# Kernel tuning notes

Measured on AMD Instinct MI355X. Metric: run time of the kernel, lower is better.

Reference implementation:

```python
import jax, jax.numpy as jnp
import numpy as np

BATCH = 16384
D = 4096  # input_features


def setup_inputs() -> dict:
    key = jax.random.key(0)
    k1, k2, k3 = jax.random.split(key, 3)
    x0 = jax.random.normal(k1, (BATCH, D), dtype=jnp.float32)
    x_cross = jax.random.normal(k2, (BATCH, D), dtype=jnp.float32)
    # RandomNormal(mean=0, stddev=sqrt(2/input_features))
    w = jax.random.normal(k3, (D,), dtype=jnp.float32) * np.float32(np.sqrt(2.0 / D))
    b = jnp.full((D,), 0.1, dtype=jnp.float32)
    return {"x0": x0, "x_cross": x_cross, "w": w, "b": b}


def reference(x0, x_cross, w, b):
    # Original: tensordot(x0[:, :, None] @ x_cross[:, None, :], w, [[-1],[0]]) + b + x_cross
    # Algebraically identical fused form (avoids the O(B*d^2) intermediate):
    #   x0 * (x_cross . w) + b + x_cross
    s = jnp.einsum("bd,d->b", x_cross, w)  # [B]
    return x0 * s[:, None] + b + x_cross
```

## Files before the change

kernel.cpp:

```cpp
#include <hip/hip_runtime.h>


constexpr int D_DIM = 4096;
constexpr int TPB   = 256;
constexpr int V4    = D_DIM / 4;
constexpr int F4PT  = V4 / TPB;

__global__ __launch_bounds__(TPB)
void cross_fused_kernel(const float* __restrict__ x0,
                        const float* __restrict__ xc,
                        const float* __restrict__ w,
                        const float* __restrict__ bias,
                        float* __restrict__ out) {
    const int row = blockIdx.x;
    const size_t base = (size_t)row * D_DIM;

    const float4* __restrict__ xc4  = (const float4*)(xc + base);
    const float4* __restrict__ x04  = (const float4*)(x0 + base);
    const float4* __restrict__ w4   = (const float4*)w;
    const float4* __restrict__ b4   = (const float4*)bias;
    float4* __restrict__       out4 = (float4*)(out + base);

    const int t = threadIdx.x;

    float4 xcv[F4PT];
    float partial = 0.0f;
#pragma unroll
    for (int i = 0; i < F4PT; ++i) {
        const int idx = t + i * TPB;
        xcv[i] = xc4[idx];
        const float4 wv = w4[idx];
        partial += xcv[i].x * wv.x + xcv[i].y * wv.y
                 + xcv[i].z * wv.z + xcv[i].w * wv.w;
    }

#pragma unroll
    for (int off = 32; off >= 1; off >>= 1)
        partial += __shfl_down(partial, off);

    __shared__ float wsum[TPB / 64];
    const int lane = t & 63, wid = t >> 6;
    if (lane == 0) wsum[wid] = partial;
    __syncthreads();
    const float s = wsum[0] + wsum[1] + wsum[2] + wsum[3];

#pragma unroll
    for (int i = 0; i < F4PT; ++i) {
        const int idx = t + i * TPB;
        const float4 x0v = x04[idx];
        const float4 bv  = b4[idx];
        float4 o;
        o.x = x0v.x * s + bv.x + xcv[i].x;
        o.y = x0v.y * s + bv.y + xcv[i].y;
        o.z = x0v.z * s + bv.z + xcv[i].z;
        o.w = x0v.w * s + bv.w + xcv[i].w;
        out4[idx] = o;
    }
}

extern "C" void kernel_launch(void* const* d_in, const int* in_sizes, int n_in,
                              void* d_out, int out_size, void* d_ws, size_t ws_size,
                              hipStream_t stream) {
    const float* x0   = (const float*)d_in[0];
    const float* xc   = (const float*)d_in[1];
    const float* w    = (const float*)d_in[2];
    const float* bias = (const float*)d_in[3];
    float* out        = (float*)d_out;

    const int rows = in_sizes[0] / D_DIM;
    cross_fused_kernel<<<rows, TPB, 0, stream>>>(x0, xc, w, bias, out);
}
```

Baseline: 141.0 us.

## Process multiple rows per block with double-buffered loads and nontemporal stores

Each block now handles eight rows and ping-pongs between two register buffers, issuing the next row's x_cross and x0 loads before storing the current row. The w and bias vectors are loaded once per block instead of once per row, and outputs use nontemporal stores. The aim is to overlap memory latency with the reduction and cut redundant weight traffic. The cost is higher register pressure, which may lower occupancy, and far fewer blocks (2048). The launch assumes the row count divides by eight.

```diff
diff --git a/kernel.cpp b/kernel.cpp
--- a/kernel.cpp
+++ b/kernel.cpp
@@ -1,10 +1,56 @@
 #include <hip/hip_runtime.h>
 
+
+typedef float f32x4 __attribute__((ext_vector_type(4)));
 
 constexpr int D_DIM = 4096;
 constexpr int TPB   = 256;
 constexpr int V4    = D_DIM / 4;
 constexpr int F4PT  = V4 / TPB;
+constexpr int NR    = 8;
+
+#define LOADROW(XCV, X0V, R)                                                  \
+    {                                                                         \
+        const f32x4* __restrict__ xc4_ = (const f32x4*)(xc + (R) * D_DIM);    \
+        const f32x4* __restrict__ x04_ = (const f32x4*)(x0 + (R) * D_DIM);    \
+        _Pragma("unroll")                                                     \
+        for (int i = 0; i < F4PT; ++i) XCV[i] = xc4_[t + i * TPB];            \
+        _Pragma("unroll")                                                     \
+        for (int i = 0; i < F4PT; ++i) X0V[i] = x04_[t + i * TPB];            \
+    }
+
+#define REDUCE(XCV, SLOT, SOUT)                                               \
+    {                                                                         \
+        float p0 = 0.f, p1 = 0.f, p2 = 0.f, p3 = 0.f;                         \
+        _Pragma("unroll")                                                     \
+        for (int i = 0; i < F4PT; ++i) {                                      \
+            p0 += XCV[i].x * wv[i].x;                                         \
+            p1 += XCV[i].y * wv[i].y;                                         \
+            p2 += XCV[i].z * wv[i].z;                                         \
+            p3 += XCV[i].w * wv[i].w;                                         \
+        }                                                                     \
+        float partial_ = (p0 + p1) + (p2 + p3);                               \
+        _Pragma("unroll")                                                     \
+        for (int off = 32; off >= 1; off >>= 1)                               \
+            partial_ += __shfl_xor(partial_, off);                            \
+        if (lane == 0) wsum[SLOT][wid] = partial_;                            \
+        __syncthreads();                                                      \
+        SOUT = wsum[SLOT][0] + wsum[SLOT][1] + wsum[SLOT][2] + wsum[SLOT][3]; \
+    }
+
+#define STOREROW(XCV, X0V, S, R)                                              \
+    {                                                                         \
+        f32x4* __restrict__ out4_ = (f32x4*)(out + (R) * D_DIM);              \
+        _Pragma("unroll")                                                     \
+        for (int i = 0; i < F4PT; ++i) {                                      \
+            f32x4 o_;                                                         \
+            o_.x = fmaf(X0V[i].x, (S), bv[i].x + XCV[i].x);                   \
+            o_.y = fmaf(X0V[i].y, (S), bv[i].y + XCV[i].y);                   \
+            o_.z = fmaf(X0V[i].z, (S), bv[i].z + XCV[i].z);                   \
+            o_.w = fmaf(X0V[i].w, (S), bv[i].w + XCV[i].w);                   \
+            __builtin_nontemporal_store(o_, &out4_[t + i * TPB]);             \
+        }                                                                     \
+    }
 
 __global__ __launch_bounds__(TPB)
 void cross_fused_kernel(const float* __restrict__ x0,
@@ -12,49 +58,37 @@
                         const float* __restrict__ w,
                         const float* __restrict__ bias,
                         float* __restrict__ out) {
-    const int row = blockIdx.x;
-    const size_t base = (size_t)row * D_DIM;
+    const int t    = threadIdx.x;
+    const int lane = t & 63;
+    const int wid  = t >> 6;
+    const size_t row0 = (size_t)blockIdx.x * NR;
 
-    const float4* __restrict__ xc4  = (const float4*)(xc + base);
-    const float4* __restrict__ x04  = (const float4*)(x0 + base);
-    const float4* __restrict__ w4   = (const float4*)w;
-    const float4* __restrict__ b4   = (const float4*)bias;
-    float4* __restrict__       out4 = (float4*)(out + base);
+    const f32x4* __restrict__ w4 = (const f32x4*)w;
+    const f32x4* __restrict__ b4 = (const f32x4*)bias;
 
-    const int t = threadIdx.x;
-
-    float4 xcv[F4PT];
-    float partial = 0.0f;
+    f32x4 wv[F4PT], bv[F4PT];
 #pragma unroll
     for (int i = 0; i < F4PT; ++i) {
-        const int idx = t + i * TPB;
-        xcv[i] = xc4[idx];
-        const float4 wv = w4[idx];
-        partial += xcv[i].x * wv.x + xcv[i].y * wv.y
-                 + xcv[i].z * wv.z + xcv[i].w * wv.w;
+        wv[i] = w4[t + i * TPB];
+        bv[i] = b4[t + i * TPB];
     }
 
-#pragma unroll
-    for (int off = 32; off >= 1; off >>= 1)
-        partial += __shfl_down(partial, off);
+    __shared__ float wsum[2][TPB / 64];
 
-    __shared__ float wsum[TPB / 64];
-    const int lane = t & 63, wid = t >> 6;
-    if (lane == 0) wsum[wid] = partial;
-    __syncthreads();
-    const float s = wsum[0] + wsum[1] + wsum[2] + wsum[3];
+    f32x4 xcA[F4PT], x0A[F4PT], xcB[F4PT], x0B[F4PT];
+    float sA, sB;
+
+    LOADROW(xcA, x0A, row0);
+    REDUCE(xcA, 0, sA);
 
 #pragma unroll
-    for (int i = 0; i < F4PT; ++i) {
-        const int idx = t + i * TPB;
-        const float4 x0v = x04[idx];
-        const float4 bv  = b4[idx];
-        float4 o;
-        o.x = x0v.x * s + bv.x + xcv[i].x;
-        o.y = x0v.y * s + bv.y + xcv[i].y;
-        o.z = x0v.z * s + bv.z + xcv[i].z;
-        o.w = x0v.w * s + bv.w + xcv[i].w;
-        out4[idx] = o;
+    for (int r = 0; r < NR; r += 2) {
+        LOADROW(xcB, x0B, row0 + r + 1);
+        STOREROW(xcA, x0A, sA, row0 + r);
+        REDUCE(xcB, 1, sB);
+        if (r + 2 < NR) LOADROW(xcA, x0A, row0 + r + 2);
+        STOREROW(xcB, x0B, sB, row0 + r + 1);
+        if (r + 2 < NR) REDUCE(xcA, 0, sA);
     }
 }
 
@@ -68,5 +102,5 @@
     float* out        = (float*)d_out;
 
     const int rows = in_sizes[0] / D_DIM;
-    cross_fused_kernel<<<rows, TPB, 0, stream>>>(x0, xc, w, bias, out);
+    cross_fused_kernel<<<rows / NR, TPB, 0, stream>>>(x0, xc, w, bias, out);
 }
```

After: 159.1 us. +12.8%, slower.
